# Kernel tuning notes

Hardware: AMD Instinct MI355X
Metric: run time of the kernel (lower is better)

## Reference

```python
import jax, jax.numpy as jnp
import numpy as np


def _gen_multi_direction_mask(w, h):
    """Numpy port of MultiDirectionPattern.generate_multi_direction_mask."""
    mask = np.zeros((8, h, w), dtype=np.float32)
    if h % 2 == 0:
        cx, cy = (w - 1) / 2.0, (h - 1) / 2.0
    else:
        cx, cy = w // 2, h // 2
    ii, jj = np.meshgrid(np.arange(w), np.arange(h))  # ii[j,i]=i, jj[j,i]=j
    deg = (np.degrees(np.arctan2(cy - jj, cx - ii)) + 180.0) % 360.0
    for i in range(8):
        d = deg.copy()
        if i == 7:
            d[d == 0] = 360.0
        m = ((d >= i * 45) & (d <= (i + 1) * 45)).astype(np.float32)
        if h % 2 != 0:
            m[int(cy), int(cx)] = 1.0
        mask[i] = m
    return mask


def setup_inputs() -> dict:
    key = jax.random.key(0)
    kx, ks = jax.random.split(key)
    B, C = 256, 2048
    x = jax.random.normal(kx, (B, C, 7, 7), dtype=jnp.float32)
    s = jax.random.uniform(ks, (B, 1, 56, 56), dtype=jnp.float32)
    feat_mask = jnp.asarray(_gen_multi_direction_mask(7, 7))   # [8,7,7]
    sal_mask = _gen_multi_direction_mask(56, 56)               # [8,56,56]
    idx_list = [np.flatnonzero(sal_mask[i].ravel()) for i in range(8)]
    n = idx_list[0].size  # 406; equal for all sectors by symmetry
    assert all(a.size == n for a in idx_list)
    sal_idx = jnp.asarray(np.stack(idx_list).astype(np.int32))  # [8,406]
    return {"x": x, "s": s, "feat_mask": feat_mask, "sal_idx": sal_idx}


def reference(x, s, feat_mask, sal_idx):
    # --- directional mean-pool over the 7x7 feature map ---
    # count of nonzero cells per direction mask, shape [8]
    count = jnp.sum(feat_mask.reshape(8, -1) != 0, axis=-1).astype(x.dtype)
    # (x.unsqueeze(2) * mask).sum(-2).sum(-1) == einsum over hw
    part = jnp.einsum('bchw,phw->bcp', x, feat_mask)   # [B,C,8]
    feat = (part / count).reshape(x.shape[0], x.shape[1], 2, 4)
    # --- directional gather from the 56x56 saliency map ---
    B, Cs = s.shape[0], s.shape[1]
    s_flat = s.reshape(B, Cs, -1)                      # [B,Cs,3136]
    gath = s_flat[:, :, sal_idx]                       # [B,Cs,8,N]
    N = gath.shape[3]
    # torch: per-sector [B, Cs*N] then stack on dim=2 -> [B, Cs*N, 8] -> [B, Cs*N, 2, 4]
    sal_feat = jnp.transpose(gath, (0, 1, 3, 2)).reshape(B, Cs * N, 2, 4)
    return feat, sal_feat
```

## Files before the change

kernel.cpp:

```cpp
#include <hip/hip_runtime.h>


#define ROWS_PER_BLOCK 256
#define KPIX 49

__global__ __launch_bounds__(256) void mdp_fused_kernel(
    const float* __restrict__ x, const float* __restrict__ s,
    const float* __restrict__ fm, const int* __restrict__ sidx,
    float* __restrict__ out, int BC, int nb1, int N, int SHW)
{
    const int tid = threadIdx.x;
    if ((int)blockIdx.x < nb1) {
        __shared__ float xs[ROWS_PER_BLOCK * KPIX];
        __shared__ float rcnt[8];

        const int r0 = blockIdx.x * ROWS_PER_BLOCK;
        const int nrows = min(ROWS_PER_BLOCK, BC - r0);

        if (tid < 8) {
            float c = 0.f;
            for (int k = 0; k < KPIX; ++k)
                c += (fm[tid * KPIX + k] != 0.f) ? 1.f : 0.f;
            rcnt[tid] = 1.0f / c;
        }

        if (nrows == ROWS_PER_BLOCK) {
            const float4* xg = (const float4*)(x + (size_t)r0 * KPIX);
            float4* xs4 = (float4*)xs;
            const int nfl4 = (ROWS_PER_BLOCK * KPIX) / 4;
            #pragma unroll 4
            for (int i = tid; i < nfl4; i += 256) xs4[i] = xg[i];
        } else {
            const int nfl = nrows * KPIX;
            const float* xg = x + (size_t)r0 * KPIX;
            for (int i = tid; i < nfl; i += 256) xs[i] = xg[i];
        }
        __syncthreads();

        const int r = r0 + tid;
        if (r < BC) {
            const float* rowp = &xs[tid * KPIX];
            float row[KPIX];
            #pragma unroll
            for (int k = 0; k < KPIX; ++k) row[k] = rowp[k];

            float rc[8];
            #pragma unroll
            for (int p = 0; p < 8; ++p) rc[p] = rcnt[p];

            float sum[8];
            #pragma unroll
            for (int p = 0; p < 8; ++p) {
                float acc = 0.f;
                #pragma unroll
                for (int k = 0; k < KPIX; ++k)
                    acc += row[k] * fm[p * KPIX + k];
                sum[p] = acc * rc[p];
            }
            float4* o = (float4*)(out + (size_t)r * 8);
            o[0] = make_float4(sum[0], sum[1], sum[2], sum[3]);
            o[1] = make_float4(sum[4], sum[5], sum[6], sum[7]);
        }
    } else {
        const int b = blockIdx.x - nb1;
        const float* srow = s + (size_t)b * SHW;
        float* o2 = out + (size_t)BC * 8 + (size_t)b * N * 8;
        const int tot = N * 8;
        for (int i = tid; i < tot; i += 256) {
            const int p = i & 7;
            const int n = i >> 3;
            o2[i] = srow[sidx[p * N + n]];
        }
    }
}

extern "C" void kernel_launch(void* const* d_in, const int* in_sizes, int n_in,
                              void* d_out, int out_size, void* d_ws, size_t ws_size,
                              hipStream_t stream) {
    const float* x    = (const float*)d_in[0];
    const float* s    = (const float*)d_in[1];
    const float* fm   = (const float*)d_in[2];
    const int*   sidx = (const int*)d_in[3];
    float* out = (float*)d_out;

    const int SHW = 3136;
    const int B   = in_sizes[1] / SHW;
    const int BC  = in_sizes[0] / KPIX;
    const int N   = in_sizes[3] / 8;

    const int nb1 = (BC + ROWS_PER_BLOCK - 1) / ROWS_PER_BLOCK;
    const int grid = nb1 + B;

    mdp_fused_kernel<<<grid, 256, 0, stream>>>(x, s, fm, sidx, out, BC, nb1, N, SHW);
}
```

Measured before the change: 171.5 us.

## Shrink blocks to single wavefronts and split saliency gather into quarters

Blocks shrink from 256 to 64 threads (one wavefront), each staging 64 rows of the 7x7 map in LDS. This cuts LDS per block from about 50KB to about 12.5KB so more blocks can be resident per CU. The per-direction counts are now computed with a wavefront ballot and popcount instead of a serial loop, and each batch's saliency gather is split across four blocks. The cost is many more small blocks and higher per-block launch overhead.

```diff
diff --git a/kernel.cpp b/kernel.cpp
--- a/kernel.cpp
+++ b/kernel.cpp
@@ -1,52 +1,48 @@
 #include <hip/hip_runtime.h>
 
 
-#define ROWS_PER_BLOCK 256
 #define KPIX 49
+#define TROWS 64
+#define TFLOATS (TROWS * KPIX)
+#define TF4 (TFLOATS / 4)
 
-__global__ __launch_bounds__(256) void mdp_fused_kernel(
+__global__ __launch_bounds__(64, 3) void mdp_fused_kernel(
     const float* __restrict__ x, const float* __restrict__ s,
     const float* __restrict__ fm, const int* __restrict__ sidx,
-    float* __restrict__ out, int BC, int nb1, int N, int SHW)
+    float* __restrict__ out, int BC, int nb1, int N, int SHW, int qper)
 {
-    const int tid = threadIdx.x;
+    const int lane = threadIdx.x;
+
     if ((int)blockIdx.x < nb1) {
-        __shared__ float xs[ROWS_PER_BLOCK * KPIX];
-        __shared__ float rcnt[8];
+        __shared__ float xs[TFLOATS];
+        const int r0 = blockIdx.x * TROWS;
 
-        const int r0 = blockIdx.x * ROWS_PER_BLOCK;
-        const int nrows = min(ROWS_PER_BLOCK, BC - r0);
-
-        if (tid < 8) {
-            float c = 0.f;
-            for (int k = 0; k < KPIX; ++k)
-                c += (fm[tid * KPIX + k] != 0.f) ? 1.f : 0.f;
-            rcnt[tid] = 1.0f / c;
+        float rc[8];
+        #pragma unroll
+        for (int p = 0; p < 8; ++p) {
+            float v = (lane < KPIX) ? fm[p * KPIX + lane] : 0.f;
+            unsigned long long bm = __ballot(v != 0.f);
+            rc[p] = 1.0f / (float)__popcll(bm);
         }
 
-        if (nrows == ROWS_PER_BLOCK) {
-            const float4* xg = (const float4*)(x + (size_t)r0 * KPIX);
-            float4* xs4 = (float4*)xs;
-            const int nfl4 = (ROWS_PER_BLOCK * KPIX) / 4;
-            #pragma unroll 4
-            for (int i = tid; i < nfl4; i += 256) xs4[i] = xg[i];
+        const float4* xg = (const float4*)(x + (size_t)r0 * KPIX);
+        float4* xs4 = (float4*)xs;
+        if (r0 + TROWS <= BC) {
+            #pragma unroll
+            for (int j = 0; j < 12; ++j) xs4[j * 64 + lane] = xg[j * 64 + lane];
+            if (lane < 16) xs4[768 + lane] = xg[768 + lane];
         } else {
-            const int nfl = nrows * KPIX;
-            const float* xg = x + (size_t)r0 * KPIX;
-            for (int i = tid; i < nfl; i += 256) xs[i] = xg[i];
+            const int nfl = (BC - r0) * KPIX;
+            const float* xgs = x + (size_t)r0 * KPIX;
+            for (int i = lane; i < nfl; i += 64) xs[i] = xgs[i];
         }
         __syncthreads();
 
-        const int r = r0 + tid;
+        const int r = r0 + lane;
         if (r < BC) {
-            const float* rowp = &xs[tid * KPIX];
             float row[KPIX];
             #pragma unroll
-            for (int k = 0; k < KPIX; ++k) row[k] = rowp[k];
-
-            float rc[8];
-            #pragma unroll
-            for (int p = 0; p < 8; ++p) rc[p] = rcnt[p];
+            for (int k = 0; k < KPIX; ++k) row[k] = xs[lane * KPIX + k];
 
             float sum[8];
             #pragma unroll
@@ -62,14 +58,15 @@
             o[1] = make_float4(sum[4], sum[5], sum[6], sum[7]);
         }
     } else {
-        const int b = blockIdx.x - nb1;
+        const int bq = blockIdx.x - nb1;
+        const int b = bq / qper, q = bq % qper;
+        const int tot = N * 8;
+        const int chunk = tot / qper;
         const float* srow = s + (size_t)b * SHW;
-        float* o2 = out + (size_t)BC * 8 + (size_t)b * N * 8;
-        const int tot = N * 8;
-        for (int i = tid; i < tot; i += 256) {
-            const int p = i & 7;
-            const int n = i >> 3;
-            o2[i] = srow[sidx[p * N + n]];
+        float* o2 = out + (size_t)BC * 8 + (size_t)b * tot + (size_t)q * chunk;
+        for (int i = lane; i < chunk; i += 64) {
+            const int e = q * chunk + i;
+            o2[i] = srow[sidx[(e & 7) * N + (e >> 3)]];
         }
     }
 }
@@ -88,8 +85,10 @@
     const int BC  = in_sizes[0] / KPIX;
     const int N   = in_sizes[3] / 8;
 
-    const int nb1 = (BC + ROWS_PER_BLOCK - 1) / ROWS_PER_BLOCK;
-    const int grid = nb1 + B;
+    const int nb1  = (BC + TROWS - 1) / TROWS;
+    const int qper = ((N * 8) % 4 == 0) ? 4 : 1;
+    const int grid = nb1 + B * qper;
 
-    mdp_fused_kernel<<<grid, 256, 0, stream>>>(x, s, fm, sidx, out, BC, nb1, N, SHW);
+    mdp_fused_kernel<<<grid, 64, 0, stream>>>(x, s, fm, sidx, out,
+                                              BC, nb1, N, SHW, qper);
 }
```

New measurement: 166.4 us. 3.0% less time.
